# Kernel tuning notes

Hardware: AMD Instinct MI355X
Metric: run time of the kernel (lower is better)

Reference implementation:

```python
import jax, jax.numpy as jnp
import numpy as np
from jax import lax

I, H, O, L = 8, 50, 6, 3
B, T = 4096, 256


def setup_inputs() -> dict:
    key = jax.random.key(0)
    ks = jax.random.split(key, 16)
    s = 1.0 / np.sqrt(H)  # PyTorch LSTM init scale
    inp = {"x": jax.random.normal(ks[0], (B, T, I), dtype=jnp.float32)}
    in_dims = [I, H, H]
    ki = 1
    for l in range(L):
        inp[f"w_ih{l}"] = jax.random.uniform(ks[ki], (4 * H, in_dims[l]), minval=-s, maxval=s); ki += 1
        inp[f"w_hh{l}"] = jax.random.uniform(ks[ki], (4 * H, H), minval=-s, maxval=s); ki += 1
        inp[f"b_ih{l}"] = jax.random.uniform(ks[ki], (4 * H,), minval=-s, maxval=s); ki += 1
        inp[f"b_hh{l}"] = jax.random.uniform(ks[ki], (4 * H,), minval=-s, maxval=s); ki += 1
    inp["w_fc"] = jax.random.uniform(ks[13], (O, H), minval=-s, maxval=s)
    inp["b_fc"] = jax.random.uniform(ks[14], (O,), minval=-s, maxval=s)
    return inp


def _lstm_layer(x, w_ih, w_hh, b_ih, b_hh):
    # x: [B, T, in]; returns [B, T, H]. PyTorch gate order: i, f, g, o.
    b = b_ih + b_hh
    pre = jnp.einsum('bti,gi->btg', x, w_ih) + b  # input projections for all steps at once
    h0 = jnp.zeros((x.shape[0], H), x.dtype)
    c0 = jnp.zeros((x.shape[0], H), x.dtype)

    def step(carry, p_t):
        h, c = carry
        gates = p_t + h @ w_hh.T
        i, f, g, o = jnp.split(gates, 4, axis=-1)
        i = jax.nn.sigmoid(i); f = jax.nn.sigmoid(f)
        g = jnp.tanh(g); o = jax.nn.sigmoid(o)
        c = f * c + i * g
        h = o * jnp.tanh(c)
        return (h, c), h

    (_, _), hs = lax.scan(step, (h0, c0), jnp.swapaxes(pre, 0, 1))  # [T, B, H]
    return jnp.swapaxes(hs, 0, 1)


def reference(x, w_ih0, w_hh0, b_ih0, b_hh0, w_ih1, w_hh1, b_ih1, b_hh1,
              w_ih2, w_hh2, b_ih2, b_hh2, w_fc, b_fc):
    h = _lstm_layer(x, w_ih0, w_hh0, b_ih0, b_hh0)
    h = _lstm_layer(h, w_ih1, w_hh1, b_ih1, b_hh1)
    h = _lstm_layer(h, w_ih2, w_hh2, b_ih2, b_hh2)
    last = h[:, -1, :]  # [B, H]
    return last @ w_fc.T + b_fc  # [B, O]
```

## Files before the change

kernel.cpp:

```cpp
#include <hip/hip_runtime.h>
#include <hip/hip_bf16.h>
#include <cstddef>


#define T_STEPS 256
#define NITER   258
#define BTOT    4096
#define NTHR    768
#define GS      128
#define BUFR    1152

typedef __attribute__((ext_vector_type(8))) _Float16 half8;
typedef __attribute__((ext_vector_type(4))) float    f32x4;

#define BAR() do { \
    asm volatile("s_waitcnt lgkmcnt(0)" ::: "memory"); \
    __builtin_amdgcn_sched_barrier(0); \
    __builtin_amdgcn_s_barrier(); \
    __builtin_amdgcn_sched_barrier(0); \
} while (0)

__device__ __forceinline__ unsigned short f2h(float x) {
    union { _Float16 h; unsigned short s; } u;
    u.h = (_Float16)x;
    return u.s;
}

__device__ __forceinline__ float cell_upd(f32x4 g, float& cst) {
    const float K2 = 2.8853900817779268f;
    float eg  = __builtin_amdgcn_exp2f(fminf(fmaxf(g[2], -126.0f), 126.0f));
    float ei  = __builtin_amdgcn_exp2f(g[0]);
    float ef  = __builtin_amdgcn_exp2f(g[1]);
    float eo  = __builtin_amdgcn_exp2f(g[3]);
    float itg = (eg - 1.0f) * __builtin_amdgcn_rcpf((1.0f + ei) * (1.0f + eg));
    float fg  = __builtin_amdgcn_rcpf(1.0f + ef);
    float c   = fmaf(fg, cst, itg);
    cst = c;
    float ec  = __builtin_amdgcn_exp2f(fminf(fmaxf(K2 * c, -126.0f), 126.0f));
    return (ec - 1.0f) * __builtin_amdgcn_rcpf((1.0f + eo) * (1.0f + ec));
}

template<bool L0M, int NT, int KS>
__device__ __forceinline__ void load_wb(int T0, int lane,
    const float* __restrict__ w_ih, const float* __restrict__ w_hh,
    const float* __restrict__ b_ih, const float* __restrict__ b_hh,
    half8 (&W)[NT][KS])
{
    const float K1 = 1.4426950408889634f, K2 = 2.8853900817779268f;
    const int m = lane & 15, kg = lane >> 4;
    #pragma unroll
    for (int q = 0; q < NT; ++q) {
        int gp = (T0 + q) * 16 + m;
        int gr = (gp < 200) ? ((gp & 3) * 50 + (gp >> 2)) : -1;
        float scale = ((gp & 3) == 2) ? K2 : -K1;
        #pragma unroll
        for (int ks = 0; ks < KS; ++ks)
            #pragma unroll
            for (int e = 0; e < 8; ++e) {
                int k = ks * 32 + kg * 8 + e;
                float v = 0.0f;
                if (gr >= 0) {
                    if (L0M) {
                        if (k < 8) v = w_ih[gr * 8 + k];
                        else if (k < 58) v = w_hh[gr * 50 + (k - 8)];
                        else if (k == 58) v = b_ih[gr] + b_hh[gr];
                    } else {
                        if (k < 50) v = w_ih[gr * 50 + k];
                        else if (k == 50) v = b_ih[gr] + b_hh[gr];
                        else if (k >= 64 && k < 114) v = w_hh[gr * 50 + (k - 64)];
                    }
                }
                W[q][ks][e] = (_Float16)(v * scale);
            }
    }
}

template<int T0, int NT, bool XST>
__device__ void role_l0(int lane, int b0, const float* __restrict__ xf,
    const float* w_ih, const float* w_hh, const float* b_ih, const float* b_hh,
    short (*H0)[BUFR])
{
    half8 W[NT][2];
    load_wb<true, NT, 2>(T0, lane, w_ih, w_hh, b_ih, b_hh, W);
    float cst[NT];
    #pragma unroll
    for (int q = 0; q < NT; ++q) cst[q] = 0.0f;
    const int b = lane & 15, kg = lane >> 4;

    for (int it = 0; it < NITER; ++it) {
        const bool stg = XST && (kg == 0) && (it + 1 < T_STEPS);
        float xs[8];
        if (stg) {
            const float* xr = &xf[((size_t)(b0 + b) * T_STEPS + (it + 1)) * 8];
            *(float4*)&xs[0] = *(const float4*)xr;
            *(float4*)&xs[4] = *(const float4*)(xr + 4);
        }
        if (it < T_STEPS) {
            const short* rb = H0[it & 1];
            short*       wb = H0[(it + 1) & 1];
            half8 A0 = *(const half8*)&rb[kg * GS + b * 8];
            half8 A1 = *(const half8*)&rb[(4 + kg) * GS + b * 8];
            f32x4 accA[NT], accB[NT];
            #pragma unroll
            for (int q = 0; q < NT; ++q) {
                accA[q] = (f32x4){0.0f, 0.0f, 0.0f, 0.0f};
                accB[q] = (f32x4){0.0f, 0.0f, 0.0f, 0.0f};
            }
            #pragma unroll
            for (int q = 0; q < NT; ++q)
                accA[q] = __builtin_amdgcn_mfma_f32_16x16x32_f16(W[q][0], A0, accA[q], 0, 0, 0);
            #pragma unroll
            for (int q = 0; q < NT; ++q)
                accB[q] = __builtin_amdgcn_mfma_f32_16x16x32_f16(W[q][1], A1, accB[q], 0, 0, 0);
            #pragma unroll
            for (int q = 0; q < NT; ++q) {
                int n = (T0 + q) * 4 + kg;
                if (n < 50) {
                    float h = cell_upd(accA[q] + accB[q], cst[q]);
                    wb[(1 + (n >> 3)) * GS + b * 8 + (n & 7)] = (short)f2h(h);
                }
            }
        }
        if (stg) {
            short hi[8];
            #pragma unroll
            for (int e = 0; e < 8; ++e) hi[e] = (short)f2h(xs[e]);
            *(half8*)&H0[(it + 1) & 1][b * 8] = *(half8*)hi;
        }
        BAR();
    }
}

template<int T0, bool LASTL>
__device__ void role_mid(int lane,
    const float* w_ih, const float* w_hh, const float* b_ih, const float* b_hh,
    short (*H0)[BUFR], short (*H1)[BUFR], short (*H2)[BUFR], float* hfp)
{
    constexpr int SKEW = LASTL ? 2 : 1;
    half8 W[3][4];
    load_wb<false, 3, 4>(T0, lane, w_ih, w_hh, b_ih, b_hh, W);
    float cst[3] = {0.0f, 0.0f, 0.0f};
    const int b = lane & 15, kg = lane >> 4;
    int m0 = 0, m1 = 2, m2 = 1;

    for (int it = 0; it < NITER; ++it) {
        int t = it - SKEW;
        if ((unsigned)t < T_STEPS) {
            const short* xsb = LASTL ? H1[m2] : H0[it & 1];
            const short* hsb = LASTL ? H2[(it + 1) & 1] : H1[m2];
            short*       wb  = LASTL ? H2[it & 1]       : H1[m1];

            half8 Ap[4];
            Ap[0] = *(const half8*)&xsb[(1 + kg) * GS + b * 8];
            Ap[1] = *(const half8*)&xsb[(5 + kg) * GS + b * 8];
            Ap[2] = *(const half8*)&hsb[(1 + kg) * GS + b * 8];
            Ap[3] = *(const half8*)&hsb[(5 + kg) * GS + b * 8];

            f32x4 accA[3], accB[3];
            #pragma unroll
            for (int q = 0; q < 3; ++q) {
                accA[q] = (f32x4){0.0f, 0.0f, 0.0f, 0.0f};
                accB[q] = (f32x4){0.0f, 0.0f, 0.0f, 0.0f};
            }
            #pragma unroll
            for (int ks = 0; ks < 4; ++ks) {
                if ((ks & 1) == 0) {
                    #pragma unroll
                    for (int q = 0; q < 3; ++q)
                        accA[q] = __builtin_amdgcn_mfma_f32_16x16x32_f16(W[q][ks], Ap[ks], accA[q], 0, 0, 0);
                } else {
                    #pragma unroll
                    for (int q = 0; q < 3; ++q)
                        accB[q] = __builtin_amdgcn_mfma_f32_16x16x32_f16(W[q][ks], Ap[ks], accB[q], 0, 0, 0);
                }
            }

            #pragma unroll
            for (int q = 0; q < 3; ++q) {
                int n = (T0 + q) * 4 + kg;
                if (n < 50) {
                    float h = cell_upd(accA[q] + accB[q], cst[q]);
                    wb[(1 + (n >> 3)) * GS + b * 8 + (n & 7)] = (short)f2h(h);
                    if (LASTL && t == T_STEPS - 1) hfp[b * 56 + n] = h;
                }
            }
        }
        BAR();
        int tmp = m2; m2 = m1; m1 = m0; m0 = tmp;
    }
}

__device__ void role_orphan(int lane,
    const float* w_ih1, const float* w_hh1, const float* b_ih1, const float* b_hh1,
    const float* w_ih2, const float* w_hh2, const float* b_ih2, const float* b_hh2,
    short (*H0)[BUFR], short (*H1)[BUFR], short (*H2)[BUFR], float* hfp)
{
    half8 W1[1][4], W2[1][4];
    load_wb<false, 1, 4>(12, lane, w_ih1, w_hh1, b_ih1, b_hh1, W1);
    load_wb<false, 1, 4>(12, lane, w_ih2, w_hh2, b_ih2, b_hh2, W2);
    float c1 = 0.0f, c2 = 0.0f;
    const int b = lane & 15, kg = lane >> 4;
    int m0 = 0, m1 = 2, m2 = 1;

    for (int it = 0; it < NITER; ++it) {
        int t1 = it - 1, t2 = it - 2;
        bool d1 = (unsigned)t1 < T_STEPS, d2 = (unsigned)t2 < T_STEPS;

        half8 A1[4], A2[4];
        if (d1) {
            const short* xsb = H0[it & 1];
            const short* hsb = H1[m2];
            A1[0] = *(const half8*)&xsb[(1 + kg) * GS + b * 8];
            A1[1] = *(const half8*)&xsb[(5 + kg) * GS + b * 8];
            A1[2] = *(const half8*)&hsb[(1 + kg) * GS + b * 8];
            A1[3] = *(const half8*)&hsb[(5 + kg) * GS + b * 8];
        }
        if (d2) {
            const short* xsb = H1[m2];
            const short* hsb = H2[(it + 1) & 1];
            A2[0] = *(const half8*)&xsb[(1 + kg) * GS + b * 8];
            A2[1] = *(const half8*)&xsb[(5 + kg) * GS + b * 8];
            A2[2] = *(const half8*)&hsb[(1 + kg) * GS + b * 8];
            A2[3] = *(const half8*)&hsb[(5 + kg) * GS + b * 8];
        }

        f32x4 a1 = (f32x4){0.0f, 0.0f, 0.0f, 0.0f};
        f32x4 a2 = (f32x4){0.0f, 0.0f, 0.0f, 0.0f};
        #pragma unroll
        for (int ks = 0; ks < 4; ++ks) {
            if (d1) a1 = __builtin_amdgcn_mfma_f32_16x16x32_f16(W1[0][ks], A1[ks], a1, 0, 0, 0);
            if (d2) a2 = __builtin_amdgcn_mfma_f32_16x16x32_f16(W2[0][ks], A2[ks], a2, 0, 0, 0);
        }

        const int n = 48 + kg;
        if (d1 && kg < 2) {
            float h = cell_upd(a1, c1);
            H1[m1][(1 + (n >> 3)) * GS + b * 8 + (n & 7)] = (short)f2h(h);
        }
        if (d2 && kg < 2) {
            float h = cell_upd(a2, c2);
            H2[it & 1][(1 + (n >> 3)) * GS + b * 8 + (n & 7)] = (short)f2h(h);
            if (t2 == T_STEPS - 1) hfp[b * 56 + n] = h;
        }
        BAR();
        int tmp = m2; m2 = m1; m1 = m0; m0 = tmp;
    }
}

__global__ __launch_bounds__(NTHR) void lstm_fused(
    const float* __restrict__ xf,
    const float* w_ih0, const float* w_hh0, const float* b_ih0, const float* b_hh0,
    const float* w_ih1, const float* w_hh1, const float* b_ih1, const float* b_hh1,
    const float* w_ih2, const float* w_hh2, const float* b_ih2, const float* b_hh2,
    const float* __restrict__ w_fc, const float* __restrict__ b_fc,
    float* __restrict__ out)
{
    __shared__ __align__(16) short H0[2][BUFR];
    __shared__ __align__(16) short H1[3][BUFR];
    __shared__ __align__(16) short H2[2][BUFR];
    __shared__ __align__(16) float hf[16 * 56];

    const int tid  = threadIdx.x;
    const int lane = tid & 63;
    const int wid  = tid >> 6;
    const int b0   = blockIdx.x * 16;

    for (int i = tid; i < 2 * BUFR; i += NTHR) { ((short*)H0)[i] = 0; ((short*)H2)[i] = 0; }
    for (int i = tid; i < 3 * BUFR; i += NTHR) ((short*)H1)[i] = 0;
    __syncthreads();

    if (tid < 80) {
        int bufi = tid >> 4, b = tid & 15;
        short* bp = (bufi < 2) ? H0[bufi] : H1[bufi - 2];
        bp[7 * GS + b * 8 + 2] = (short)0x3C00;
    }
    if (tid < 16) {
        int b = tid;
        #pragma unroll
        for (int j = 0; j < 8; ++j) {
            float v = xf[((size_t)(b0 + b) * T_STEPS + 0) * 8 + j];
            H0[0][b * 8 + j] = (short)f2h(v);
        }
    }
    __syncthreads();

    if      (wid == 0)  role_l0<0, 5, false>(lane, b0, xf, w_ih0, w_hh0, b_ih0, b_hh0, H0);
    else if (wid == 1)  role_l0<5, 4, false>(lane, b0, xf, w_ih0, w_hh0, b_ih0, b_hh0, H0);
    else if (wid == 2)  role_l0<9, 4, true >(lane, b0, xf, w_ih0, w_hh0, b_ih0, b_hh0, H0);
    else if (wid == 3)  role_mid<0, false>(lane, w_ih1, w_hh1, b_ih1, b_hh1, H0, H1, H2, nullptr);
    else if (wid == 4)  role_mid<3, false>(lane, w_ih1, w_hh1, b_ih1, b_hh1, H0, H1, H2, nullptr);
    else if (wid == 5)  role_mid<6, false>(lane, w_ih1, w_hh1, b_ih1, b_hh1, H0, H1, H2, nullptr);
    else if (wid == 6)  role_mid<9, false>(lane, w_ih1, w_hh1, b_ih1, b_hh1, H0, H1, H2, nullptr);
    else if (wid == 7)  role_mid<0, true >(lane, w_ih2, w_hh2, b_ih2, b_hh2, H0, H1, H2, hf);
    else if (wid == 8)  role_mid<3, true >(lane, w_ih2, w_hh2, b_ih2, b_hh2, H0, H1, H2, hf);
    else if (wid == 9)  role_mid<6, true >(lane, w_ih2, w_hh2, b_ih2, b_hh2, H0, H1, H2, hf);
    else if (wid == 10) role_mid<9, true >(lane, w_ih2, w_hh2, b_ih2, b_hh2, H0, H1, H2, hf);
    else                role_orphan(lane,
                            w_ih1, w_hh1, b_ih1, b_hh1,
                            w_ih2, w_hh2, b_ih2, b_hh2,
                            H0, H1, H2, hf);

    __syncthreads();

    if (tid < 96) {
        int b = tid / 6, o = tid - b * 6;
        float a = b_fc[o];
        #pragma unroll
        for (int n = 0; n < 50; ++n)
            a = fmaf(w_fc[o * 50 + n], hf[b * 56 + n], a);
        out[(size_t)(b0 + b) * 6 + o] = a;
    }
}

extern "C" void kernel_launch(void* const* d_in, const int* in_sizes, int n_in,
                              void* d_out, int out_size, void* d_ws, size_t ws_size,
                              hipStream_t stream) {
    (void)in_sizes; (void)n_in; (void)d_ws; (void)ws_size; (void)out_size;

    const float* x     = (const float*)d_in[0];
    const float* w_ih0 = (const float*)d_in[1];
    const float* w_hh0 = (const float*)d_in[2];
    const float* b_ih0 = (const float*)d_in[3];
    const float* b_hh0 = (const float*)d_in[4];
    const float* w_ih1 = (const float*)d_in[5];
    const float* w_hh1 = (const float*)d_in[6];
    const float* b_ih1 = (const float*)d_in[7];
    const float* b_hh1 = (const float*)d_in[8];
    const float* w_ih2 = (const float*)d_in[9];
    const float* w_hh2 = (const float*)d_in[10];
    const float* b_ih2 = (const float*)d_in[11];
    const float* b_hh2 = (const float*)d_in[12];
    const float* w_fc  = (const float*)d_in[13];
    const float* b_fc  = (const float*)d_in[14];
    float* out = (float*)d_out;

    lstm_fused<<<dim3(BTOT / 16), dim3(NTHR), 0, stream>>>(
        x, w_ih0, w_hh0, b_ih0, b_hh0, w_ih1, w_hh1, b_ih1, b_hh1,
        w_ih2, w_hh2, b_ih2, b_hh2, w_fc, b_fc, out);
}
```

Before: 256.4 us.

## Give each wave one gate tile across all three layers instead of per-layer roles

Replaces the per-layer wave specialization (3 waves for layer 0, 4 for layer 1, 4 for layer 2, plus an orphan wave) with 13 uniform waves. Each wave owns one 16-row gate tile and computes that tile for all three layers every iteration. This balances MFMA and transcendental work evenly across waves and removes the imbalance where layer-0 waves did 5 tiles while others did 3. The cost is one extra wave in the workgroup, more weight registers per wave (10 half8 vectors), and wave 12 doing mostly idle gate work alongside x staging.

After: 342.2 us. 1.33x slower.

```diff
diff --git a/kernel.cpp b/kernel.cpp
--- a/kernel.cpp
+++ b/kernel.cpp
@@ -6,7 +6,7 @@
 #define T_STEPS 256
 #define NITER   258
 #define BTOT    4096
-#define NTHR    768
+#define NTHR    832
 #define GS      128
 #define BUFR    1152
 
@@ -40,211 +40,53 @@
     return (ec - 1.0f) * __builtin_amdgcn_rcpf((1.0f + eo) * (1.0f + ec));
 }
 
-template<bool L0M, int NT, int KS>
-__device__ __forceinline__ void load_wb(int T0, int lane,
+__device__ __forceinline__ void load_w0(int T0, int lane,
     const float* __restrict__ w_ih, const float* __restrict__ w_hh,
     const float* __restrict__ b_ih, const float* __restrict__ b_hh,
-    half8 (&W)[NT][KS])
+    half8 (&W)[2])
 {
     const float K1 = 1.4426950408889634f, K2 = 2.8853900817779268f;
     const int m = lane & 15, kg = lane >> 4;
+    int gp = T0 * 16 + m;
+    int gr = (gp < 200) ? ((gp & 3) * 50 + (gp >> 2)) : -1;
+    float scale = ((gp & 3) == 2) ? K2 : -K1;
     #pragma unroll
-    for (int q = 0; q < NT; ++q) {
-        int gp = (T0 + q) * 16 + m;
-        int gr = (gp < 200) ? ((gp & 3) * 50 + (gp >> 2)) : -1;
-        float scale = ((gp & 3) == 2) ? K2 : -K1;
-        #pragma unroll
-        for (int ks = 0; ks < KS; ++ks)
-            #pragma unroll
-            for (int e = 0; e < 8; ++e) {
-                int k = ks * 32 + kg * 8 + e;
-                float v = 0.0f;
-                if (gr >= 0) {
-                    if (L0M) {
-                        if (k < 8) v = w_ih[gr * 8 + k];
-                        else if (k < 58) v = w_hh[gr * 50 + (k - 8)];
-                        else if (k == 58) v = b_ih[gr] + b_hh[gr];
-                    } else {
-                        if (k < 50) v = w_ih[gr * 50 + k];
-                        else if (k == 50) v = b_ih[gr] + b_hh[gr];
-                        else if (k >= 64 && k < 114) v = w_hh[gr * 50 + (k - 64)];
-                    }
-                }
-                W[q][ks][e] = (_Float16)(v * scale);
+    for (int ks = 0; ks < 2; ++ks)
+        #pragma unroll
+        for (int e = 0; e < 8; ++e) {
+            int k = ks * 32 + kg * 8 + e;
+            float v = 0.0f;
+            if (gr >= 0) {
+                if (k < 8) v = w_ih[gr * 8 + k];
+                else if (k < 58) v = w_hh[gr * 50 + (k - 8)];
+                else if (k == 58) v = b_ih[gr] + b_hh[gr];
             }
-    }
-}
-
-template<int T0, int NT, bool XST>
-__device__ void role_l0(int lane, int b0, const float* __restrict__ xf,
-    const float* w_ih, const float* w_hh, const float* b_ih, const float* b_hh,
-    short (*H0)[BUFR])
+            W[ks][e] = (_Float16)(v * scale);
+        }
+}
+__device__ __forceinline__ void load_wm(int T0, int lane,
+    const float* __restrict__ w_ih, const float* __restrict__ w_hh,
+    const float* __restrict__ b_ih, const float* __restrict__ b_hh,
+    half8 (&W)[4])
 {
-    half8 W[NT][2];
-    load_wb<true, NT, 2>(T0, lane, w_ih, w_hh, b_ih, b_hh, W);
-    float cst[NT];
+    const float K1 = 1.4426950408889634f, K2 = 2.8853900817779268f;
+    const int m = lane & 15, kg = lane >> 4;
+    int gp = T0 * 16 + m;
+    int gr = (gp < 200) ? ((gp & 3) * 50 + (gp >> 2)) : -1;
+    float scale = ((gp & 3) == 2) ? K2 : -K1;
     #pragma unroll
-    for (int q = 0; q < NT; ++q) cst[q] = 0.0f;
-    const int b = lane & 15, kg = lane >> 4;
-
-    for (int it = 0; it < NITER; ++it) {
-        const bool stg = XST && (kg == 0) && (it + 1 < T_STEPS);
-        float xs[8];
-        if (stg) {
-            const float* xr = &xf[((size_t)(b0 + b) * T_STEPS + (it + 1)) * 8];
-            *(float4*)&xs[0] = *(const float4*)xr;
-            *(float4*)&xs[4] = *(const float4*)(xr + 4);
-        }
-        if (it < T_STEPS) {
-            const short* rb = H0[it & 1];
-            short*       wb = H0[(it + 1) & 1];
-            half8 A0 = *(const half8*)&rb[kg * GS + b * 8];
-            half8 A1 = *(const half8*)&rb[(4 + kg) * GS + b * 8];
-            f32x4 accA[NT], accB[NT];
-            #pragma unroll
-            for (int q = 0; q < NT; ++q) {
-                accA[q] = (f32x4){0.0f, 0.0f, 0.0f, 0.0f};
-                accB[q] = (f32x4){0.0f, 0.0f, 0.0f, 0.0f};
+    for (int ks = 0; ks < 4; ++ks)
+        #pragma unroll
+        for (int e = 0; e < 8; ++e) {
+            int k = ks * 32 + kg * 8 + e;
+            float v = 0.0f;
+            if (gr >= 0) {
+                if (k < 50) v = w_ih[gr * 50 + k];
+                else if (k == 50) v = b_ih[gr] + b_hh[gr];
+                else if (k >= 64 && k < 114) v = w_hh[gr * 50 + (k - 64)];
             }
-            #pragma unroll
-            for (int q = 0; q < NT; ++q)
-                accA[q] = __builtin_amdgcn_mfma_f32_16x16x32_f16(W[q][0], A0, accA[q], 0, 0, 0);
-            #pragma unroll
-            for (int q = 0; q < NT; ++q)
-                accB[q] = __builtin_amdgcn_mfma_f32_16x16x32_f16(W[q][1], A1, accB[q], 0, 0, 0);
-            #pragma unroll
-            for (int q = 0; q < NT; ++q) {
-                int n = (T0 + q) * 4 + kg;
-                if (n < 50) {
-                    float h = cell_upd(accA[q] + accB[q], cst[q]);
-                    wb[(1 + (n >> 3)) * GS + b * 8 + (n & 7)] = (short)f2h(h);
-                }
-            }
-        }
-        if (stg) {
-            short hi[8];
-            #pragma unroll
-            for (int e = 0; e < 8; ++e) hi[e] = (short)f2h(xs[e]);
-            *(half8*)&H0[(it + 1) & 1][b * 8] = *(half8*)hi;
-        }
-        BAR();
-    }
-}
-
-template<int T0, bool LASTL>
-__device__ void role_mid(int lane,
-    const float* w_ih, const float* w_hh, const float* b_ih, const float* b_hh,
-    short (*H0)[BUFR], short (*H1)[BUFR], short (*H2)[BUFR], float* hfp)
-{
-    constexpr int SKEW = LASTL ? 2 : 1;
-    half8 W[3][4];
-    load_wb<false, 3, 4>(T0, lane, w_ih, w_hh, b_ih, b_hh, W);
-    float cst[3] = {0.0f, 0.0f, 0.0f};
-    const int b = lane & 15, kg = lane >> 4;
-    int m0 = 0, m1 = 2, m2 = 1;
-
-    for (int it = 0; it < NITER; ++it) {
-        int t = it - SKEW;
-        if ((unsigned)t < T_STEPS) {
-            const short* xsb = LASTL ? H1[m2] : H0[it & 1];
-            const short* hsb = LASTL ? H2[(it + 1) & 1] : H1[m2];
-            short*       wb  = LASTL ? H2[it & 1]       : H1[m1];
-
-            half8 Ap[4];
-            Ap[0] = *(const half8*)&xsb[(1 + kg) * GS + b * 8];
-            Ap[1] = *(const half8*)&xsb[(5 + kg) * GS + b * 8];
-            Ap[2] = *(const half8*)&hsb[(1 + kg) * GS + b * 8];
-            Ap[3] = *(const half8*)&hsb[(5 + kg) * GS + b * 8];
-
-            f32x4 accA[3], accB[3];
-            #pragma unroll
-            for (int q = 0; q < 3; ++q) {
-                accA[q] = (f32x4){0.0f, 0.0f, 0.0f, 0.0f};
-                accB[q] = (f32x4){0.0f, 0.0f, 0.0f, 0.0f};
-            }
-            #pragma unroll
-            for (int ks = 0; ks < 4; ++ks) {
-                if ((ks & 1) == 0) {
-                    #pragma unroll
-                    for (int q = 0; q < 3; ++q)
-                        accA[q] = __builtin_amdgcn_mfma_f32_16x16x32_f16(W[q][ks], Ap[ks], accA[q], 0, 0, 0);
-                } else {
-                    #pragma unroll
-                    for (int q = 0; q < 3; ++q)
-                        accB[q] = __builtin_amdgcn_mfma_f32_16x16x32_f16(W[q][ks], Ap[ks], accB[q], 0, 0, 0);
-                }
-            }
-
-            #pragma unroll
-            for (int q = 0; q < 3; ++q) {
-                int n = (T0 + q) * 4 + kg;
-                if (n < 50) {
-                    float h = cell_upd(accA[q] + accB[q], cst[q]);
-                    wb[(1 + (n >> 3)) * GS + b * 8 + (n & 7)] = (short)f2h(h);
-                    if (LASTL && t == T_STEPS - 1) hfp[b * 56 + n] = h;
-                }
-            }
-        }
-        BAR();
-        int tmp = m2; m2 = m1; m1 = m0; m0 = tmp;
-    }
-}
-
-__device__ void role_orphan(int lane,
-    const float* w_ih1, const float* w_hh1, const float* b_ih1, const float* b_hh1,
-    const float* w_ih2, const float* w_hh2, const float* b_ih2, const float* b_hh2,
-    short (*H0)[BUFR], short (*H1)[BUFR], short (*H2)[BUFR], float* hfp)
-{
-    half8 W1[1][4], W2[1][4];
-    load_wb<false, 1, 4>(12, lane, w_ih1, w_hh1, b_ih1, b_hh1, W1);
-    load_wb<false, 1, 4>(12, lane, w_ih2, w_hh2, b_ih2, b_hh2, W2);
-    float c1 = 0.0f, c2 = 0.0f;
-    const int b = lane & 15, kg = lane >> 4;
-    int m0 = 0, m1 = 2, m2 = 1;
-
-    for (int it = 0; it < NITER; ++it) {
-        int t1 = it - 1, t2 = it - 2;
-        bool d1 = (unsigned)t1 < T_STEPS, d2 = (unsigned)t2 < T_STEPS;
-
-        half8 A1[4], A2[4];
-        if (d1) {
-            const short* xsb = H0[it & 1];
-            const short* hsb = H1[m2];
-            A1[0] = *(const half8*)&xsb[(1 + kg) * GS + b * 8];
-            A1[1] = *(const half8*)&xsb[(5 + kg) * GS + b * 8];
-            A1[2] = *(const half8*)&hsb[(1 + kg) * GS + b * 8];
-            A1[3] = *(const half8*)&hsb[(5 + kg) * GS + b * 8];
-        }
-        if (d2) {
-            const short* xsb = H1[m2];
-            const short* hsb = H2[(it + 1) & 1];
-            A2[0] = *(const half8*)&xsb[(1 + kg) * GS + b * 8];
-            A2[1] = *(const half8*)&xsb[(5 + kg) * GS + b * 8];
-            A2[2] = *(const half8*)&hsb[(1 + kg) * GS + b * 8];
-            A2[3] = *(const half8*)&hsb[(5 + kg) * GS + b * 8];
-        }
-
-        f32x4 a1 = (f32x4){0.0f, 0.0f, 0.0f, 0.0f};
-        f32x4 a2 = (f32x4){0.0f, 0.0f, 0.0f, 0.0f};
-        #pragma unroll
-        for (int ks = 0; ks < 4; ++ks) {
-            if (d1) a1 = __builtin_amdgcn_mfma_f32_16x16x32_f16(W1[0][ks], A1[ks], a1, 0, 0, 0);
-            if (d2) a2 = __builtin_amdgcn_mfma_f32_16x16x32_f16(W2[0][ks], A2[ks], a2, 0, 0, 0);
-        }
-
-        const int n = 48 + kg;
-        if (d1 && kg < 2) {
-            float h = cell_upd(a1, c1);
-            H1[m1][(1 + (n >> 3)) * GS + b * 8 + (n & 7)] = (short)f2h(h);
-        }
-        if (d2 && kg < 2) {
-            float h = cell_upd(a2, c2);
-            H2[it & 1][(1 + (n >> 3)) * GS + b * 8 + (n & 7)] = (short)f2h(h);
-            if (t2 == T_STEPS - 1) hfp[b * 56 + n] = h;
-        }
-        BAR();
-        int tmp = m2; m2 = m1; m1 = m0; m0 = tmp;
-    }
+            W[ks][e] = (_Float16)(v * scale);
+        }
 }
 
 __global__ __launch_bounds__(NTHR) void lstm_fused(
@@ -284,31 +126,110 @@
     }
     __syncthreads();
 
-    if      (wid == 0)  role_l0<0, 5, false>(lane, b0, xf, w_ih0, w_hh0, b_ih0, b_hh0, H0);
-    else if (wid == 1)  role_l0<5, 4, false>(lane, b0, xf, w_ih0, w_hh0, b_ih0, b_hh0, H0);
-    else if (wid == 2)  role_l0<9, 4, true >(lane, b0, xf, w_ih0, w_hh0, b_ih0, b_hh0, H0);
-    else if (wid == 3)  role_mid<0, false>(lane, w_ih1, w_hh1, b_ih1, b_hh1, H0, H1, H2, nullptr);
-    else if (wid == 4)  role_mid<3, false>(lane, w_ih1, w_hh1, b_ih1, b_hh1, H0, H1, H2, nullptr);
-    else if (wid == 5)  role_mid<6, false>(lane, w_ih1, w_hh1, b_ih1, b_hh1, H0, H1, H2, nullptr);
-    else if (wid == 6)  role_mid<9, false>(lane, w_ih1, w_hh1, b_ih1, b_hh1, H0, H1, H2, nullptr);
-    else if (wid == 7)  role_mid<0, true >(lane, w_ih2, w_hh2, b_ih2, b_hh2, H0, H1, H2, hf);
-    else if (wid == 8)  role_mid<3, true >(lane, w_ih2, w_hh2, b_ih2, b_hh2, H0, H1, H2, hf);
-    else if (wid == 9)  role_mid<6, true >(lane, w_ih2, w_hh2, b_ih2, b_hh2, H0, H1, H2, hf);
-    else if (wid == 10) role_mid<9, true >(lane, w_ih2, w_hh2, b_ih2, b_hh2, H0, H1, H2, hf);
-    else                role_orphan(lane,
-                            w_ih1, w_hh1, b_ih1, b_hh1,
-                            w_ih2, w_hh2, b_ih2, b_hh2,
-                            H0, H1, H2, hf);
+    const int  T0  = wid;
+    const bool XW  = (wid == 12);
+    const int  b   = lane & 15, kg = lane >> 4;
+    const bool gok = (T0 < 12) || (kg < 2);
+    const int  n   = T0 * 4 + kg;
+    const int  wof = (1 + (n >> 3)) * GS + b * 8 + (n & 7);
+
+    half8 W0[2], W1[4], W2[4];
+    load_w0(T0, lane, w_ih0, w_hh0, b_ih0, b_hh0, W0);
+    load_wm(T0, lane, w_ih1, w_hh1, b_ih1, b_hh1, W1);
+    load_wm(T0, lane, w_ih2, w_hh2, b_ih2, b_hh2, W2);
+    float c0 = 0.0f, c1 = 0.0f, c2 = 0.0f;
+    int m0 = 0, m1 = 2, m2 = 1;
+
+    for (int it = 0; it < NITER; ++it) {
+        const int t1 = it - 1, t2 = it - 2;
+        const bool d0 = it < T_STEPS;
+        const bool d1 = (unsigned)t1 < T_STEPS;
+        const bool d2 = (unsigned)t2 < T_STEPS;
+
+        const bool stg = XW && (kg == 0) && (it + 1 < T_STEPS);
+        float4 xa, xb;
+        if (stg) {
+            const float* xr = &xf[((size_t)(b0 + b) * T_STEPS + (it + 1)) * 8];
+            xa = *(const float4*)xr;
+            xb = *(const float4*)(xr + 4);
+        }
+
+        half8 A00, A01, A1x0, A1x1, A1h0, A1h1, A2x0, A2x1, A2h0, A2h1;
+        if (d0) {
+            const short* rb = H0[it & 1];
+            A00 = *(const half8*)&rb[kg * GS + b * 8];
+            A01 = *(const half8*)&rb[(4 + kg) * GS + b * 8];
+        }
+        if (d1) {
+            const short* xp = H0[it & 1];
+            const short* hp = H1[m2];
+            A1x0 = *(const half8*)&xp[(1 + kg) * GS + b * 8];
+            A1x1 = *(const half8*)&xp[(5 + kg) * GS + b * 8];
+            A1h0 = *(const half8*)&hp[(1 + kg) * GS + b * 8];
+            A1h1 = *(const half8*)&hp[(5 + kg) * GS + b * 8];
+        }
+        if (d2) {
+            const short* xp = H1[m2];
+            const short* hp = H2[(it + 1) & 1];
+            A2x0 = *(const half8*)&xp[(1 + kg) * GS + b * 8];
+            A2x1 = *(const half8*)&xp[(5 + kg) * GS + b * 8];
+            A2h0 = *(const half8*)&hp[(1 + kg) * GS + b * 8];
+            A2h1 = *(const half8*)&hp[(5 + kg) * GS + b * 8];
+        }
+
+        f32x4 a0  = (f32x4){0.0f, 0.0f, 0.0f, 0.0f};
+        f32x4 a1A = a0, a1B = a0, a2A = a0, a2B = a0;
+        if (d0) {
+            a0 = __builtin_amdgcn_mfma_f32_16x16x32_f16(W0[0], A00, a0, 0, 0, 0);
+            a0 = __builtin_amdgcn_mfma_f32_16x16x32_f16(W0[1], A01, a0, 0, 0, 0);
+        }
+        if (d1) {
+            a1A = __builtin_amdgcn_mfma_f32_16x16x32_f16(W1[0], A1x0, a1A, 0, 0, 0);
+            a1B = __builtin_amdgcn_mfma_f32_16x16x32_f16(W1[1], A1x1, a1B, 0, 0, 0);
+            a1A = __builtin_amdgcn_mfma_f32_16x16x32_f16(W1[2], A1h0, a1A, 0, 0, 0);
+            a1B = __builtin_amdgcn_mfma_f32_16x16x32_f16(W1[3], A1h1, a1B, 0, 0, 0);
+        }
+        if (d2) {
+            a2A = __builtin_amdgcn_mfma_f32_16x16x32_f16(W2[0], A2x0, a2A, 0, 0, 0);
+            a2B = __builtin_amdgcn_mfma_f32_16x16x32_f16(W2[1], A2x1, a2B, 0, 0, 0);
+            a2A = __builtin_amdgcn_mfma_f32_16x16x32_f16(W2[2], A2h0, a2A, 0, 0, 0);
+            a2B = __builtin_amdgcn_mfma_f32_16x16x32_f16(W2[3], A2h1, a2B, 0, 0, 0);
+        }
+
+        if (d0 && gok) {
+            float h = cell_upd(a0, c0);
+            H0[(it + 1) & 1][wof] = (short)f2h(h);
+        }
+        if (d1 && gok) {
+            float h = cell_upd(a1A + a1B, c1);
+            H1[m1][wof] = (short)f2h(h);
+        }
+        if (d2 && gok) {
+            float h = cell_upd(a2A + a2B, c2);
+            H2[it & 1][wof] = (short)f2h(h);
+            if (t2 == T_STEPS - 1) hf[b * 56 + n] = h;
+        }
+        if (stg) {
+            short hi[8];
+            hi[0] = (short)f2h(xa.x); hi[1] = (short)f2h(xa.y);
+            hi[2] = (short)f2h(xa.z); hi[3] = (short)f2h(xa.w);
+            hi[4] = (short)f2h(xb.x); hi[5] = (short)f2h(xb.y);
+            hi[6] = (short)f2h(xb.z); hi[7] = (short)f2h(xb.w);
+            *(half8*)&H0[(it + 1) & 1][b * 8] = *(half8*)hi;
+        }
+        BAR();
+        int tmp = m2; m2 = m1; m1 = m0; m0 = tmp;
+    }
 
     __syncthreads();
 
     if (tid < 96) {
-        int b = tid / 6, o = tid - b * 6;
+        int bb = tid / 6, o = tid - bb * 6;
         float a = b_fc[o];
         #pragma unroll
-        for (int n = 0; n < 50; ++n)
-            a = fmaf(w_fc[o * 50 + n], hf[b * 56 + n], a);
-        out[(size_t)(b0 + b) * 6 + o] = a;
+        for (int u = 0; u < 50; ++u)
+            a = fmaf(w_fc[o * 50 + u], hf[bb * 56 + u], a);
+        out[(size_t)(b0 + bb) * 6 + o] = a;
     }
 }
 
```
